# Optimization experiments

Hardware: AMD Instinct MI355X
Metric: run time of the kernel (lower is better)

The kernel has to match this reference:

```python
import jax, jax.numpy as jnp
import numpy as np

FEAT = 1024
HID = 512
DK = 256
N = 8192
KMAX = 8
K_LIST = (2, 4, 8)


def setup_inputs() -> dict:
    key = jax.random.key(0)
    ks = jax.random.split(key, 10)
    def glorot(k, shape):
        lim = np.sqrt(6.0 / (shape[0] + shape[1]))
        return jax.random.uniform(k, shape, jnp.float32, -lim, lim)
    return {
        "input_tensor": jax.random.normal(ks[0], (N, FEAT), jnp.float32),
        "sp_matrix": jax.random.randint(ks[1], (N, KMAX + 1), 0, N, jnp.int64 if jax.config.jax_enable_x64 else jnp.int32),
        "W1": glorot(ks[2], (FEAT, HID)),
        "b1": jnp.zeros((HID,), jnp.float32),
        "Wq": glorot(ks[3], (HID, DK)),
        "Wk": glorot(ks[4], (HID, DK)),
        "Wv": glorot(ks[5], (HID, DK)),
        "bv": jnp.zeros((DK,), jnp.float32),
        "Wout": glorot(ks[6], (DK, 2)),
        "bout": jnp.zeros((2,), jnp.float32),
    }


def reference(input_tensor, sp_matrix, W1, b1, Wq, Wk, Wv, bv, Wout, bout):
    # fc1: Dense(512, relu)
    dense = jax.nn.relu(input_tensor @ W1 + b1)            # [n, 512]
    # CustomAttention: scaled QK^T over the whole bag
    q = dense @ Wq                                          # [n, 256]
    k = dense @ Wk                                          # [n, 256]
    attn = (q @ k.T) / jnp.sqrt(jnp.float32(DK))            # [n, n]
    value = dense @ Wv + bv                                 # [n, 256]
    pools = []
    for kk in K_LIST:
        idx = sp_matrix[:, : kk + 1]                        # [n, kk+1]
        # sparse adjacency * attention, row-sum == gather attn[i, idx[i,j]] and sum over j
        a_raw = jnp.take_along_axis(attn, idx, axis=1).sum(axis=1)  # [n]
        alpha = jax.nn.softmax(a_raw)                       # [n]
        pools.append(alpha[:, None] * value)                # [n, 256]
    spp = jnp.concatenate(pools, axis=0)                    # [3n, 256]
    # Last_Sigmoid (subtyping=True): sum-pool -> dense -> softmax
    logits = spp.sum(axis=0, keepdims=True) @ Wout + bout   # [1, 2]
    return jax.nn.softmax(logits, axis=-1)
```

## Files before the change

kernel.cpp:

```cpp
#include <hip/hip_runtime.h>
#include <hip/hip_bf16.h>
#include <math.h>

#define FEAT 1024
#define HID  512
#define DK   256
#define NROWS 8192

typedef __attribute__((ext_vector_type(8))) short short8;
typedef __attribute__((ext_vector_type(4))) float floatx4;

__device__ __forceinline__ unsigned short f2bf(float x) {
    union { float f; unsigned u; } u;
    u.f = x;
    unsigned r = u.u;
    r += 0x7fffu + ((r >> 16) & 1u);
    return (unsigned short)(r >> 16);
}
__device__ __forceinline__ float bf2f(unsigned short x) {
    union { unsigned u; float f; } u;
    u.u = ((unsigned)x) << 16;
    return u.f;
}

__device__ __forceinline__ void gld_lds16(const unsigned short* g, unsigned short* l) {
    __builtin_amdgcn_global_load_lds(
        (__attribute__((address_space(1))) void*)(void*)g,
        (__attribute__((address_space(3))) void*)l,
        16, 0, 0);
}

__global__ __launch_bounds__(256) void prep_kernel(
    const float* __restrict__ X, const float* __restrict__ W1,
    const float* __restrict__ Wq, const float* __restrict__ Wk,
    const float* __restrict__ Wv,
    unsigned short* __restrict__ Xb, unsigned short* __restrict__ W1T,
    unsigned short* __restrict__ WqT, unsigned short* __restrict__ WkT,
    unsigned short* __restrict__ WvT,
    float* __restrict__ P, float* __restrict__ Z)
{
    const int b = blockIdx.x;
    const int tid = threadIdx.x;

    if (b == 0) {
        for (int i = tid; i < 3 * DK; i += 256) P[i] = 0.f;
        if (tid < 3) Z[tid] = 0.f;
    }
    if (b < 8192) {
        int i = b * 256 + tid;
        float4 v = ((const float4*)X)[i];
        ushort4 o;
        o.x = f2bf(v.x); o.y = f2bf(v.y); o.z = f2bf(v.z); o.w = f2bf(v.w);
        ((ushort4*)Xb)[i] = o;
        return;
    }
    int t = b - 8192;
    const float* in; unsigned short* outp; int K, N, tn, tk;
    if (t < 512) {
        in = W1; outp = W1T; K = FEAT; N = HID; tn = t & 15; tk = t >> 4;
    } else {
        t -= 512;
        int z = t >> 7, r = t & 127;
        K = HID; N = DK; tn = r & 7; tk = r >> 3;
        in   = (z == 0) ? Wq  : (z == 1) ? Wk  : Wv;
        outp = (z == 0) ? WqT : (z == 1) ? WkT : WvT;
    }
    __shared__ float tt[32][33];
    const int tx = tid & 31, ty = tid >> 5;
    const int n0 = tn * 32, k0 = tk * 32;
    #pragma unroll
    for (int i2 = ty; i2 < 32; i2 += 8)
        tt[i2][tx] = in[(size_t)(k0 + i2) * N + (n0 + tx)];
    __syncthreads();
    #pragma unroll
    for (int i2 = ty; i2 < 32; i2 += 8)
        outp[(size_t)(n0 + i2) * K + (k0 + tx)] = f2bf(tt[tx][i2]);
}

__global__ __launch_bounds__(256) void gemm_mfma(
    const unsigned short* __restrict__ A,
    const unsigned short* __restrict__ BT0, const unsigned short* __restrict__ BT1,
    const unsigned short* __restrict__ BT2,
    const float* __restrict__ bias0, const float* __restrict__ bias1,
    const float* __restrict__ bias2,
    unsigned short* __restrict__ C0, unsigned short* __restrict__ C1,
    unsigned short* __restrict__ C2,
    int N, int K, int relu)
{
    const unsigned short* BT = (blockIdx.z == 0) ? BT0 : (blockIdx.z == 1) ? BT1 : BT2;
    const float* bias        = (blockIdx.z == 0) ? bias0 : (blockIdx.z == 1) ? bias1 : bias2;
    unsigned short* C        = (blockIdx.z == 0) ? C0 : (blockIdx.z == 1) ? C1 : C2;

    __shared__ __align__(16) unsigned short As[64 * 32];
    __shared__ __align__(16) unsigned short Bs[128 * 32];

    const int tid  = threadIdx.x;
    const int lane = tid & 63;
    const int wid  = tid >> 6;
    const int wm = wid >> 1, wn = wid & 1;
    const int m0 = blockIdx.y * 64, n0 = blockIdx.x * 128;

    const int rowA = tid >> 2, gA = tid & 3;
    const int sgA = gA ^ ((rowA >> 1) & 3);
    const unsigned short* Ap = A + (size_t)(m0 + rowA) * K + sgA * 8;

    const int idx0 = tid, idx1 = tid + 256;
    const int rowB0 = idx0 >> 2, gB0 = idx0 & 3;
    const int rowB1 = idx1 >> 2, gB1 = idx1 & 3;
    const int sgB0 = gB0 ^ ((rowB0 >> 1) & 3);
    const int sgB1 = gB1 ^ ((rowB1 >> 1) & 3);
    const unsigned short* Bp0 = BT + (size_t)(n0 + rowB0) * K + sgB0 * 8;
    const unsigned short* Bp1 = BT + (size_t)(n0 + rowB1) * K + sgB1 * 8;

    char* AsB = (char*)As;
    char* BsB = (char*)Bs;
    const int ldsA  = wid * 1024;
    const int ldsB0 = wid * 1024;
    const int ldsB1 = wid * 1024 + 4096;

    const int gr = lane >> 4;
    int aoff[2], boff[4];
    #pragma unroll
    for (int i = 0; i < 2; ++i) {
        int ra = wm * 32 + i * 16 + (lane & 15);
        aoff[i] = ra * 64 + ((gr ^ ((ra >> 1) & 3)) * 16);
    }
    #pragma unroll
    for (int j = 0; j < 4; ++j) {
        int rb = wn * 64 + j * 16 + (lane & 15);
        boff[j] = rb * 64 + ((gr ^ ((rb >> 1) & 3)) * 16);
    }

    floatx4 acc[2][4];
    #pragma unroll
    for (int i = 0; i < 2; ++i)
        #pragma unroll
        for (int j = 0; j < 4; ++j)
            acc[i][j] = (floatx4){0.f, 0.f, 0.f, 0.f};

    for (int kt = 0; kt < K; kt += 32) {
        gld_lds16(Ap  + kt, (unsigned short*)(AsB + ldsA));
        gld_lds16(Bp0 + kt, (unsigned short*)(BsB + ldsB0));
        gld_lds16(Bp1 + kt, (unsigned short*)(BsB + ldsB1));
        __syncthreads();

        short8 af[2], bfr[4];
        #pragma unroll
        for (int i = 0; i < 2; ++i) af[i] = *(const short8*)(AsB + aoff[i]);
        #pragma unroll
        for (int j = 0; j < 4; ++j) bfr[j] = *(const short8*)(BsB + boff[j]);
        #pragma unroll
        for (int i = 0; i < 2; ++i)
            #pragma unroll
            for (int j = 0; j < 4; ++j)
                acc[i][j] = __builtin_amdgcn_mfma_f32_16x16x32_bf16(
                    af[i], bfr[j], acc[i][j], 0, 0, 0);
        __syncthreads();
    }

    #pragma unroll
    for (int i = 0; i < 2; ++i) {
        int rbase = m0 + wm * 32 + i * 16 + (lane >> 4) * 4;
        #pragma unroll
        for (int j = 0; j < 4; ++j) {
            int c = n0 + wn * 64 + j * 16 + (lane & 15);
            float bb = bias ? bias[c] : 0.f;
            #pragma unroll
            for (int r = 0; r < 4; ++r) {
                float v = acc[i][j][r] + bb;
                if (relu) v = fmaxf(v, 0.f);
                C[(size_t)(rbase + r) * N + c] = f2bf(v);
            }
        }
    }
}

__global__ __launch_bounds__(256) void gather_attn(
    const unsigned short* __restrict__ Q, const unsigned short* __restrict__ Kmat,
    const int* __restrict__ sp, float* __restrict__ a_raw,
    float* __restrict__ mxp)
{
    const int lane = threadIdx.x & 63;
    const int wid  = threadIdx.x >> 6;
    const int i = blockIdx.x * 4 + wid;

    ushort4 qr = *(const ushort4*)(Q + (size_t)i * DK + lane * 4);
    float4 q = make_float4(bf2f(qr.x), bf2f(qr.y), bf2f(qr.z), bf2f(qr.w));
    float4 ks = make_float4(0.f, 0.f, 0.f, 0.f);

    float mloc[3];
    int sel = 0;
    #pragma unroll
    for (int j = 0; j <= 8; ++j) {
        int r = sp[i * 9 + j];
        ushort4 kr = *(const ushort4*)(Kmat + (size_t)r * DK + lane * 4);
        ks.x += bf2f(kr.x); ks.y += bf2f(kr.y);
        ks.z += bf2f(kr.z); ks.w += bf2f(kr.w);
        if (j == 2 || j == 4 || j == 8) {
            float d = q.x * ks.x + q.y * ks.y + q.z * ks.z + q.w * ks.w;
            #pragma unroll
            for (int off = 32; off; off >>= 1) d += __shfl_xor(d, off);
            d *= 0.0625f;
            if (lane == 0) a_raw[sel * NROWS + i] = d;
            mloc[sel] = d;
            ++sel;
        }
    }

    __shared__ float sm[3][4];
    if (lane == 0) {
        sm[0][wid] = mloc[0]; sm[1][wid] = mloc[1]; sm[2][wid] = mloc[2];
    }
    __syncthreads();
    if (threadIdx.x < 3) {
        float m = fmaxf(fmaxf(sm[threadIdx.x][0], sm[threadIdx.x][1]),
                        fmaxf(sm[threadIdx.x][2], sm[threadIdx.x][3]));
        mxp[threadIdx.x * 2048 + blockIdx.x] = m;
    }
}

#define RPB 64
__global__ __launch_bounds__(256) void pool_kernel(
    const float* __restrict__ a_raw, const float* __restrict__ mxp,
    const unsigned short* __restrict__ V, float* __restrict__ P,
    float* __restrict__ Z)
{
    const int r0 = blockIdx.x * RPB;
    const int t = threadIdx.x;

    __shared__ float red[3][256];
    __shared__ float e[3][RPB];

    float m0 = -INFINITY, m1 = -INFINITY, m2 = -INFINITY;
    #pragma unroll
    for (int k = 0; k < 8; ++k) {
        int idx = t + k * 256;
        m0 = fmaxf(m0, mxp[idx]);
        m1 = fmaxf(m1, mxp[2048 + idx]);
        m2 = fmaxf(m2, mxp[4096 + idx]);
    }
    red[0][t] = m0; red[1][t] = m1; red[2][t] = m2;
    __syncthreads();
    for (int st = 128; st; st >>= 1) {
        if (t < st) {
            red[0][t] = fmaxf(red[0][t], red[0][t + st]);
            red[1][t] = fmaxf(red[1][t], red[1][t + st]);
            red[2][t] = fmaxf(red[2][t], red[2][t + st]);
        }
        __syncthreads();
    }
    m0 = red[0][0]; m1 = red[1][0]; m2 = red[2][0];

    float z0 = 0.f, z1 = 0.f, z2 = 0.f;
    if (t < RPB) {
        z0 = expf(a_raw[0 * NROWS + r0 + t] - m0);
        z1 = expf(a_raw[1 * NROWS + r0 + t] - m1);
        z2 = expf(a_raw[2 * NROWS + r0 + t] - m2);
        e[0][t] = z0; e[1][t] = z1; e[2][t] = z2;
    }
    __syncthreads();

    float a0 = 0.f, a1 = 0.f, a2 = 0.f;
    for (int r = 0; r < RPB; ++r) {
        float v = bf2f(V[(size_t)(r0 + r) * DK + t]);
        a0 = fmaf(e[0][r], v, a0);
        a1 = fmaf(e[1][r], v, a1);
        a2 = fmaf(e[2][r], v, a2);
    }
    atomicAdd(&P[0 * DK + t], a0);
    atomicAdd(&P[1 * DK + t], a1);
    atomicAdd(&P[2 * DK + t], a2);

    #pragma unroll
    for (int off = 32; off; off >>= 1) {
        z0 += __shfl_xor(z0, off); z1 += __shfl_xor(z1, off); z2 += __shfl_xor(z2, off);
    }
    if (t == 0) {
        atomicAdd(&Z[0], z0); atomicAdd(&Z[1], z1); atomicAdd(&Z[2], z2);
    }
}

__global__ __launch_bounds__(256) void final_kernel(
    const float* __restrict__ P, const float* __restrict__ Z,
    const float* __restrict__ Wout, const float* __restrict__ bout,
    float* __restrict__ out)
{
    const int t = threadIdx.x;
    float s = P[t] / Z[0] + P[DK + t] / Z[1] + P[2 * DK + t] / Z[2];
    __shared__ float s0[256], s1[256];
    s0[t] = s * Wout[t * 2 + 0];
    s1[t] = s * Wout[t * 2 + 1];
    __syncthreads();
    for (int st = 128; st; st >>= 1) {
        if (t < st) { s0[t] += s0[t + st]; s1[t] += s1[t + st]; }
        __syncthreads();
    }
    if (t == 0) {
        float a = s0[0] + bout[0], b = s1[0] + bout[1];
        float mm = fmaxf(a, b);
        float ea = expf(a - mm), eb = expf(b - mm);
        float inv = 1.f / (ea + eb);
        out[0] = ea * inv;
        out[1] = eb * inv;
    }
}

extern "C" void kernel_launch(void* const* d_in, const int* in_sizes, int n_in,
                              void* d_out, int out_size, void* d_ws, size_t ws_size,
                              hipStream_t stream)
{
    const float* X    = (const float*)d_in[0];
    const int*   sp   = (const int*)  d_in[1];
    const float* W1   = (const float*)d_in[2];
    const float* b1   = (const float*)d_in[3];
    const float* Wq   = (const float*)d_in[4];
    const float* Wk   = (const float*)d_in[5];
    const float* Wv   = (const float*)d_in[6];
    const float* bv   = (const float*)d_in[7];
    const float* Wout = (const float*)d_in[8];
    const float* bout = (const float*)d_in[9];
    float* out = (float*)d_out;

    char* w = (char*)d_ws;
    unsigned short* dense_b = (unsigned short*)(w);
    unsigned short* W1T     = (unsigned short*)(w +  8388608);
    unsigned short* WqT     = (unsigned short*)(w +  9437184);
    unsigned short* WkT     = (unsigned short*)(w +  9699328);
    unsigned short* WvT     = (unsigned short*)(w +  9961472);
    float* a_raw            = (float*)(w + 10223616);
    float* P                = (float*)(w + 10321920);
    float* Z                = P + 3 * DK;
    float* mxp              = (float*)(w + 10330112);
    unsigned short* Qb      = (unsigned short*)(w + 10485760);
    unsigned short* Kb      = (unsigned short*)(w + 14680064);
    unsigned short* Vb      = (unsigned short*)(w + 18874368);
    unsigned short* Xb      = (unsigned short*)(w + 10485760);

    prep_kernel<<<8192 + 512 + 384, 256, 0, stream>>>(
        X, W1, Wq, Wk, Wv, Xb, W1T, WqT, WkT, WvT, P, Z);

    gemm_mfma<<<dim3(HID / 128, NROWS / 64, 1), 256, 0, stream>>>(
        Xb, W1T, nullptr, nullptr, b1, nullptr, nullptr,
        dense_b, nullptr, nullptr, HID, FEAT, 1);

    gemm_mfma<<<dim3(DK / 128, NROWS / 64, 3), 256, 0, stream>>>(
        dense_b, WqT, WkT, WvT, nullptr, nullptr, bv,
        Qb, Kb, Vb, DK, HID, 0);

    gather_attn<<<NROWS / 4, 256, 0, stream>>>(Qb, Kb, sp, a_raw, mxp);
    pool_kernel<<<NROWS / RPB, 256, 0, stream>>>(a_raw, mxp, Vb, P, Z);
    final_kernel<<<1, 256, 0, stream>>>(P, Z, Wout, bout, out);
}
```

Measured before the change: 71.54 us.

## Fuse X bf16 cast into GEMM, double-buffer LDS, fold final kernel into pool

Removes the separate pass that converts X to bf16. The first GEMM now reads fp32 X directly and converts it to bf16 while staging into LDS, which saves a full write and read of the bf16 copy. The GEMM now double-buffers its LDS tiles so the next tile's loads overlap the current tile's MFMAs, with one barrier per iteration. The final reduction kernel is folded into pool_kernel through a last-block atomic counter, saving a launch at the cost of threadfence and atomic reads.

```diff
diff --git a/kernel.cpp b/kernel.cpp
--- a/kernel.cpp
+++ b/kernel.cpp
@@ -30,14 +30,21 @@
         16, 0, 0);
 }
 
+__device__ __forceinline__ short8 cast8(float4 a, float4 b) {
+    short8 r;
+    r[0] = (short)f2bf(a.x); r[1] = (short)f2bf(a.y);
+    r[2] = (short)f2bf(a.z); r[3] = (short)f2bf(a.w);
+    r[4] = (short)f2bf(b.x); r[5] = (short)f2bf(b.y);
+    r[6] = (short)f2bf(b.z); r[7] = (short)f2bf(b.w);
+    return r;
+}
+
 __global__ __launch_bounds__(256) void prep_kernel(
-    const float* __restrict__ X, const float* __restrict__ W1,
-    const float* __restrict__ Wq, const float* __restrict__ Wk,
-    const float* __restrict__ Wv,
-    unsigned short* __restrict__ Xb, unsigned short* __restrict__ W1T,
-    unsigned short* __restrict__ WqT, unsigned short* __restrict__ WkT,
-    unsigned short* __restrict__ WvT,
-    float* __restrict__ P, float* __restrict__ Z)
+    const float* __restrict__ W1, const float* __restrict__ Wq,
+    const float* __restrict__ Wk, const float* __restrict__ Wv,
+    unsigned short* __restrict__ W1T, unsigned short* __restrict__ WqT,
+    unsigned short* __restrict__ WkT, unsigned short* __restrict__ WvT,
+    float* __restrict__ P, float* __restrict__ Z, unsigned* __restrict__ counter)
 {
     const int b = blockIdx.x;
     const int tid = threadIdx.x;
@@ -45,16 +52,10 @@
     if (b == 0) {
         for (int i = tid; i < 3 * DK; i += 256) P[i] = 0.f;
         if (tid < 3) Z[tid] = 0.f;
-    }
-    if (b < 8192) {
-        int i = b * 256 + tid;
-        float4 v = ((const float4*)X)[i];
-        ushort4 o;
-        o.x = f2bf(v.x); o.y = f2bf(v.y); o.z = f2bf(v.z); o.w = f2bf(v.w);
-        ((ushort4*)Xb)[i] = o;
-        return;
-    }
-    int t = b - 8192;
+        if (tid == 0) *counter = 0u;
+    }
+
+    int t = b;
     const float* in; unsigned short* outp; int K, N, tn, tk;
     if (t < 512) {
         in = W1; outp = W1T; K = FEAT; N = HID; tn = t & 15; tk = t >> 4;
@@ -77,8 +78,9 @@
         outp[(size_t)(n0 + i2) * K + (k0 + tx)] = f2bf(tt[tx][i2]);
 }
 
+template<int A_F32>
 __global__ __launch_bounds__(256) void gemm_mfma(
-    const unsigned short* __restrict__ A,
+    const void* __restrict__ Av,
     const unsigned short* __restrict__ BT0, const unsigned short* __restrict__ BT1,
     const unsigned short* __restrict__ BT2,
     const float* __restrict__ bias0, const float* __restrict__ bias1,
@@ -91,8 +93,8 @@
     const float* bias        = (blockIdx.z == 0) ? bias0 : (blockIdx.z == 1) ? bias1 : bias2;
     unsigned short* C        = (blockIdx.z == 0) ? C0 : (blockIdx.z == 1) ? C1 : C2;
 
-    __shared__ __align__(16) unsigned short As[64 * 32];
-    __shared__ __align__(16) unsigned short Bs[128 * 32];
+    __shared__ __align__(16) unsigned short As[2][64 * 32];
+    __shared__ __align__(16) unsigned short Bs[2][128 * 32];
 
     const int tid  = threadIdx.x;
     const int lane = tid & 63;
@@ -102,22 +104,17 @@
 
     const int rowA = tid >> 2, gA = tid & 3;
     const int sgA = gA ^ ((rowA >> 1) & 3);
-    const unsigned short* Ap = A + (size_t)(m0 + rowA) * K + sgA * 8;
-
-    const int idx0 = tid, idx1 = tid + 256;
-    const int rowB0 = idx0 >> 2, gB0 = idx0 & 3;
+    const float*          ApF = (const float*)Av + (size_t)(m0 + rowA) * K + gA * 8;
+    const unsigned short* ApB = (const unsigned short*)Av + (size_t)(m0 + rowA) * K + sgA * 8;
+
+    const int idx1 = tid + 256;
+    const int rowB0 = tid >> 2,  gB0 = tid & 3;
     const int rowB1 = idx1 >> 2, gB1 = idx1 & 3;
     const int sgB0 = gB0 ^ ((rowB0 >> 1) & 3);
     const int sgB1 = gB1 ^ ((rowB1 >> 1) & 3);
     const unsigned short* Bp0 = BT + (size_t)(n0 + rowB0) * K + sgB0 * 8;
     const unsigned short* Bp1 = BT + (size_t)(n0 + rowB1) * K + sgB1 * 8;
 
-    char* AsB = (char*)As;
-    char* BsB = (char*)Bs;
-    const int ldsA  = wid * 1024;
-    const int ldsB0 = wid * 1024;
-    const int ldsB1 = wid * 1024 + 4096;
-
     const int gr = lane >> 4;
     int aoff[2], boff[4];
     #pragma unroll
@@ -138,24 +135,66 @@
         for (int j = 0; j < 4; ++j)
             acc[i][j] = (floatx4){0.f, 0.f, 0.f, 0.f};
 
-    for (int kt = 0; kt < K; kt += 32) {
-        gld_lds16(Ap  + kt, (unsigned short*)(AsB + ldsA));
-        gld_lds16(Bp0 + kt, (unsigned short*)(BsB + ldsB0));
-        gld_lds16(Bp1 + kt, (unsigned short*)(BsB + ldsB1));
-        __syncthreads();
-
+    if (A_F32) {
+        float4 a0 = *(const float4*)(ApF);
+        float4 a1 = *(const float4*)(ApF + 4);
+        gld_lds16(Bp0, (unsigned short*)((char*)Bs[0] + wid * 1024));
+        gld_lds16(Bp1, (unsigned short*)((char*)Bs[0] + wid * 1024 + 4096));
+        *(short8*)((char*)As[0] + rowA * 64 + sgA * 16) = cast8(a0, a1);
+    } else {
+        gld_lds16(ApB, (unsigned short*)((char*)As[0] + wid * 1024));
+        gld_lds16(Bp0, (unsigned short*)((char*)Bs[0] + wid * 1024));
+        gld_lds16(Bp1, (unsigned short*)((char*)Bs[0] + wid * 1024 + 4096));
+    }
+    __syncthreads();
+
+    int cur = 0;
+    for (int kt = 32; kt < K; kt += 32) {
+        float4 na, nb;
+        if (A_F32) {
+            na = *(const float4*)(ApF + kt);
+            nb = *(const float4*)(ApF + kt + 4);
+        } else {
+            gld_lds16(ApB + kt, (unsigned short*)((char*)As[cur ^ 1] + wid * 1024));
+        }
+        gld_lds16(Bp0 + kt, (unsigned short*)((char*)Bs[cur ^ 1] + wid * 1024));
+        gld_lds16(Bp1 + kt, (unsigned short*)((char*)Bs[cur ^ 1] + wid * 1024 + 4096));
+
+        const char* AsC = (const char*)As[cur];
+        const char* BsC = (const char*)Bs[cur];
         short8 af[2], bfr[4];
         #pragma unroll
-        for (int i = 0; i < 2; ++i) af[i] = *(const short8*)(AsB + aoff[i]);
-        #pragma unroll
-        for (int j = 0; j < 4; ++j) bfr[j] = *(const short8*)(BsB + boff[j]);
+        for (int i = 0; i < 2; ++i) af[i] = *(const short8*)(AsC + aoff[i]);
+        #pragma unroll
+        for (int j = 0; j < 4; ++j) bfr[j] = *(const short8*)(BsC + boff[j]);
         #pragma unroll
         for (int i = 0; i < 2; ++i)
             #pragma unroll
             for (int j = 0; j < 4; ++j)
                 acc[i][j] = __builtin_amdgcn_mfma_f32_16x16x32_bf16(
                     af[i], bfr[j], acc[i][j], 0, 0, 0);
+
+        if (A_F32)
+            *(short8*)((char*)As[cur ^ 1] + rowA * 64 + sgA * 16) = cast8(na, nb);
+
         __syncthreads();
+        cur ^= 1;
+    }
+
+    {
+        const char* AsC = (const char*)As[cur];
+        const char* BsC = (const char*)Bs[cur];
+        short8 af[2], bfr[4];
+        #pragma unroll
+        for (int i = 0; i < 2; ++i) af[i] = *(const short8*)(AsC + aoff[i]);
+        #pragma unroll
+        for (int j = 0; j < 4; ++j) bfr[j] = *(const short8*)(BsC + boff[j]);
+        #pragma unroll
+        for (int i = 0; i < 2; ++i)
+            #pragma unroll
+            for (int j = 0; j < 4; ++j)
+                acc[i][j] = __builtin_amdgcn_mfma_f32_16x16x32_bf16(
+                    af[i], bfr[j], acc[i][j], 0, 0, 0);
     }
 
     #pragma unroll
@@ -223,13 +262,17 @@
 __global__ __launch_bounds__(256) void pool_kernel(
     const float* __restrict__ a_raw, const float* __restrict__ mxp,
     const unsigned short* __restrict__ V, float* __restrict__ P,
-    float* __restrict__ Z)
+    float* __restrict__ Z, unsigned* __restrict__ counter,
+    const float* __restrict__ Wout, const float* __restrict__ bout,
+    float* __restrict__ out)
 {
     const int r0 = blockIdx.x * RPB;
     const int t = threadIdx.x;
 
     __shared__ float red[3][256];
     __shared__ float e[3][RPB];
+    __shared__ unsigned rank;
+    __shared__ float zz[3];
 
     float m0 = -INFINITY, m1 = -INFINITY, m2 = -INFINITY;
     #pragma unroll
@@ -278,30 +321,36 @@
     if (t == 0) {
         atomicAdd(&Z[0], z0); atomicAdd(&Z[1], z1); atomicAdd(&Z[2], z2);
     }
-}
-
-__global__ __launch_bounds__(256) void final_kernel(
-    const float* __restrict__ P, const float* __restrict__ Z,
-    const float* __restrict__ Wout, const float* __restrict__ bout,
-    float* __restrict__ out)
-{
-    const int t = threadIdx.x;
-    float s = P[t] / Z[0] + P[DK + t] / Z[1] + P[2 * DK + t] / Z[2];
-    __shared__ float s0[256], s1[256];
-    s0[t] = s * Wout[t * 2 + 0];
-    s1[t] = s * Wout[t * 2 + 1];
-    __syncthreads();
-    for (int st = 128; st; st >>= 1) {
-        if (t < st) { s0[t] += s0[t + st]; s1[t] += s1[t + st]; }
+
+    __threadfence();
+    if (t == 0) rank = atomicAdd(counter, 1u);
+    __syncthreads();
+    if (rank == gridDim.x - 1) {
+        __threadfence();
+        if (t < 3) zz[t] = atomicAdd(&Z[t], 0.0f);
         __syncthreads();
-    }
-    if (t == 0) {
-        float a = s0[0] + bout[0], b = s1[0] + bout[1];
-        float mm = fmaxf(a, b);
-        float ea = expf(a - mm), eb = expf(b - mm);
-        float inv = 1.f / (ea + eb);
-        out[0] = ea * inv;
-        out[1] = eb * inv;
+        float p0 = atomicAdd(&P[0 * DK + t], 0.0f);
+        float p1 = atomicAdd(&P[1 * DK + t], 0.0f);
+        float p2 = atomicAdd(&P[2 * DK + t], 0.0f);
+        float s = p0 / zz[0] + p1 / zz[1] + p2 / zz[2];
+        red[0][t] = s * Wout[t * 2 + 0];
+        red[1][t] = s * Wout[t * 2 + 1];
+        __syncthreads();
+        for (int st = 128; st; st >>= 1) {
+            if (t < st) {
+                red[0][t] += red[0][t + st];
+                red[1][t] += red[1][t + st];
+            }
+            __syncthreads();
+        }
+        if (t == 0) {
+            float a = red[0][0] + bout[0], b = red[1][0] + bout[1];
+            float mm = fmaxf(a, b);
+            float ea = expf(a - mm), eb = expf(b - mm);
+            float inv = 1.f / (ea + eb);
+            out[0] = ea * inv;
+            out[1] = eb * inv;
+        }
     }
 }
 
@@ -330,24 +379,24 @@
     float* a_raw            = (float*)(w + 10223616);
     float* P                = (float*)(w + 10321920);
     float* Z                = P + 3 * DK;
+    unsigned* counter       = (unsigned*)(Z + 3);
     float* mxp              = (float*)(w + 10330112);
     unsigned short* Qb      = (unsigned short*)(w + 10485760);
     unsigned short* Kb      = (unsigned short*)(w + 14680064);
     unsigned short* Vb      = (unsigned short*)(w + 18874368);
-    unsigned short* Xb      = (unsigned short*)(w + 10485760);
-
-    prep_kernel<<<8192 + 512 + 384, 256, 0, stream>>>(
-        X, W1, Wq, Wk, Wv, Xb, W1T, WqT, WkT, WvT, P, Z);
-
-    gemm_mfma<<<dim3(HID / 128, NROWS / 64, 1), 256, 0, stream>>>(
-        Xb, W1T, nullptr, nullptr, b1, nullptr, nullptr,
+
+    prep_kernel<<<896, 256, 0, stream>>>(
+        W1, Wq, Wk, Wv, W1T, WqT, WkT, WvT, P, Z, counter);
+
+    gemm_mfma<1><<<dim3(HID / 128, NROWS / 64, 1), 256, 0, stream>>>(
+        X, W1T, nullptr, nullptr, b1, nullptr, nullptr,
         dense_b, nullptr, nullptr, HID, FEAT, 1);
 
-    gemm_mfma<<<dim3(DK / 128, NROWS / 64, 3), 256, 0, stream>>>(
+    gemm_mfma<0><<<dim3(DK / 128, NROWS / 64, 3), 256, 0, stream>>>(
         dense_b, WqT, WkT, WvT, nullptr, nullptr, bv,
         Qb, Kb, Vb, DK, HID, 0);
 
     gather_attn<<<NROWS / 4, 256, 0, stream>>>(Qb, Kb, sp, a_raw, mxp);
-    pool_kernel<<<NROWS / RPB, 256, 0, stream>>>(a_raw, mxp, Vb, P, Z);
-    final_kernel<<<1, 256, 0, stream>>>(P, Z, Wout, bout, out);
-}
+    pool_kernel<<<NROWS / RPB, 256, 0, stream>>>(
+        a_raw, mxp, Vb, P, Z, counter, Wout, bout, out);
+}
```

Measured after the change: 89.22 us. 1.25x slower.

## Remap GEMM blocks to XCD-aware 1D grid and fuse final reduction into pool

Applied to the files above, without the earlier changes.

Each GEMM launch becomes a 1D grid whose block index is decoded so that blocks sharing an A row-tile land on the same XCD (blockIdx & 7). The goal is better L2 reuse of the A operand across N tiles and Q/K/V outputs. Separately, final_kernel is removed: pool_kernel uses an atomic completion counter so the last block reads P and Z and computes the output softmax, saving one kernel launch. The last-block pattern depends on fences and atomic reads for correctness, and it adds a serial tail to one block.

```diff
diff --git a/kernel.cpp b/kernel.cpp
--- a/kernel.cpp
+++ b/kernel.cpp
@@ -37,7 +37,7 @@
     unsigned short* __restrict__ Xb, unsigned short* __restrict__ W1T,
     unsigned short* __restrict__ WqT, unsigned short* __restrict__ WkT,
     unsigned short* __restrict__ WvT,
-    float* __restrict__ P, float* __restrict__ Z)
+    float* __restrict__ P, float* __restrict__ Z, unsigned* __restrict__ counter)
 {
     const int b = blockIdx.x;
     const int tid = threadIdx.x;
@@ -45,6 +45,7 @@
     if (b == 0) {
         for (int i = tid; i < 3 * DK; i += 256) P[i] = 0.f;
         if (tid < 3) Z[tid] = 0.f;
+        if (tid == 0) *counter = 0u;
     }
     if (b < 8192) {
         int i = b * 256 + tid;
@@ -85,11 +86,20 @@
     const float* __restrict__ bias2,
     unsigned short* __restrict__ C0, unsigned short* __restrict__ C1,
     unsigned short* __restrict__ C2,
-    int N, int K, int relu)
-{
-    const unsigned short* BT = (blockIdx.z == 0) ? BT0 : (blockIdx.z == 1) ? BT1 : BT2;
-    const float* bias        = (blockIdx.z == 0) ? bias0 : (blockIdx.z == 1) ? bias1 : bias2;
-    unsigned short* C        = (blockIdx.z == 0) ? C0 : (blockIdx.z == 1) ? C1 : C2;
+    int N, int K, int relu, int nbx, int nz)
+{
+    const int nbxe = nbx * nz;
+    const int xcd = blockIdx.x & 7;
+    const int j   = blockIdx.x >> 3;
+    const int grp = j / nbxe;
+    const int sub = j - grp * nbxe;
+    const int by  = xcd + (grp << 3);
+    const int bx  = sub % nbx;
+    const int z   = sub / nbx;
+
+    const unsigned short* BT = (z == 0) ? BT0 : (z == 1) ? BT1 : BT2;
+    const float* bias        = (z == 0) ? bias0 : (z == 1) ? bias1 : bias2;
+    unsigned short* C        = (z == 0) ? C0 : (z == 1) ? C1 : C2;
 
     __shared__ __align__(16) unsigned short As[64 * 32];
     __shared__ __align__(16) unsigned short Bs[128 * 32];
@@ -98,14 +108,14 @@
     const int lane = tid & 63;
     const int wid  = tid >> 6;
     const int wm = wid >> 1, wn = wid & 1;
-    const int m0 = blockIdx.y * 64, n0 = blockIdx.x * 128;
+    const int m0 = by * 64, n0 = bx * 128;
 
     const int rowA = tid >> 2, gA = tid & 3;
     const int sgA = gA ^ ((rowA >> 1) & 3);
     const unsigned short* Ap = A + (size_t)(m0 + rowA) * K + sgA * 8;
 
-    const int idx0 = tid, idx1 = tid + 256;
-    const int rowB0 = idx0 >> 2, gB0 = idx0 & 3;
+    const int idx1 = tid + 256;
+    const int rowB0 = tid >> 2,  gB0 = tid & 3;
     const int rowB1 = idx1 >> 2, gB1 = idx1 & 3;
     const int sgB0 = gB0 ^ ((rowB0 >> 1) & 3);
     const int sgB1 = gB1 ^ ((rowB1 >> 1) & 3);
@@ -126,17 +136,17 @@
         aoff[i] = ra * 64 + ((gr ^ ((ra >> 1) & 3)) * 16);
     }
     #pragma unroll
-    for (int j = 0; j < 4; ++j) {
-        int rb = wn * 64 + j * 16 + (lane & 15);
-        boff[j] = rb * 64 + ((gr ^ ((rb >> 1) & 3)) * 16);
+    for (int jj = 0; jj < 4; ++jj) {
+        int rb = wn * 64 + jj * 16 + (lane & 15);
+        boff[jj] = rb * 64 + ((gr ^ ((rb >> 1) & 3)) * 16);
     }
 
     floatx4 acc[2][4];
     #pragma unroll
     for (int i = 0; i < 2; ++i)
         #pragma unroll
-        for (int j = 0; j < 4; ++j)
-            acc[i][j] = (floatx4){0.f, 0.f, 0.f, 0.f};
+        for (int jj = 0; jj < 4; ++jj)
+            acc[i][jj] = (floatx4){0.f, 0.f, 0.f, 0.f};
 
     for (int kt = 0; kt < K; kt += 32) {
         gld_lds16(Ap  + kt, (unsigned short*)(AsB + ldsA));
@@ -148,13 +158,13 @@
         #pragma unroll
         for (int i = 0; i < 2; ++i) af[i] = *(const short8*)(AsB + aoff[i]);
         #pragma unroll
-        for (int j = 0; j < 4; ++j) bfr[j] = *(const short8*)(BsB + boff[j]);
+        for (int jj = 0; jj < 4; ++jj) bfr[jj] = *(const short8*)(BsB + boff[jj]);
         #pragma unroll
         for (int i = 0; i < 2; ++i)
             #pragma unroll
-            for (int j = 0; j < 4; ++j)
-                acc[i][j] = __builtin_amdgcn_mfma_f32_16x16x32_bf16(
-                    af[i], bfr[j], acc[i][j], 0, 0, 0);
+            for (int jj = 0; jj < 4; ++jj)
+                acc[i][jj] = __builtin_amdgcn_mfma_f32_16x16x32_bf16(
+                    af[i], bfr[jj], acc[i][jj], 0, 0, 0);
         __syncthreads();
     }
 
@@ -162,12 +172,12 @@
     for (int i = 0; i < 2; ++i) {
         int rbase = m0 + wm * 32 + i * 16 + (lane >> 4) * 4;
         #pragma unroll
-        for (int j = 0; j < 4; ++j) {
-            int c = n0 + wn * 64 + j * 16 + (lane & 15);
+        for (int jj = 0; jj < 4; ++jj) {
+            int c = n0 + wn * 64 + jj * 16 + (lane & 15);
             float bb = bias ? bias[c] : 0.f;
             #pragma unroll
             for (int r = 0; r < 4; ++r) {
-                float v = acc[i][j][r] + bb;
+                float v = acc[i][jj][r] + bb;
                 if (relu) v = fmaxf(v, 0.f);
                 C[(size_t)(rbase + r) * N + c] = f2bf(v);
             }
@@ -223,13 +233,17 @@
 __global__ __launch_bounds__(256) void pool_kernel(
     const float* __restrict__ a_raw, const float* __restrict__ mxp,
     const unsigned short* __restrict__ V, float* __restrict__ P,
-    float* __restrict__ Z)
+    float* __restrict__ Z, unsigned* __restrict__ counter,
+    const float* __restrict__ Wout, const float* __restrict__ bout,
+    float* __restrict__ out)
 {
     const int r0 = blockIdx.x * RPB;
     const int t = threadIdx.x;
 
     __shared__ float red[3][256];
     __shared__ float e[3][RPB];
+    __shared__ unsigned rank;
+    __shared__ float zz[3];
 
     float m0 = -INFINITY, m1 = -INFINITY, m2 = -INFINITY;
     #pragma unroll
@@ -278,30 +292,36 @@
     if (t == 0) {
         atomicAdd(&Z[0], z0); atomicAdd(&Z[1], z1); atomicAdd(&Z[2], z2);
     }
-}
-
-__global__ __launch_bounds__(256) void final_kernel(
-    const float* __restrict__ P, const float* __restrict__ Z,
-    const float* __restrict__ Wout, const float* __restrict__ bout,
-    float* __restrict__ out)
-{
-    const int t = threadIdx.x;
-    float s = P[t] / Z[0] + P[DK + t] / Z[1] + P[2 * DK + t] / Z[2];
-    __shared__ float s0[256], s1[256];
-    s0[t] = s * Wout[t * 2 + 0];
-    s1[t] = s * Wout[t * 2 + 1];
-    __syncthreads();
-    for (int st = 128; st; st >>= 1) {
-        if (t < st) { s0[t] += s0[t + st]; s1[t] += s1[t + st]; }
-        __syncthreads();
-    }
-    if (t == 0) {
-        float a = s0[0] + bout[0], b = s1[0] + bout[1];
-        float mm = fmaxf(a, b);
-        float ea = expf(a - mm), eb = expf(b - mm);
-        float inv = 1.f / (ea + eb);
-        out[0] = ea * inv;
-        out[1] = eb * inv;
+
+    __threadfence();
+    if (t == 0) rank = atomicAdd(counter, 1u);
+    __syncthreads();
+    if (rank == gridDim.x - 1) {
+        __threadfence();
+        if (t < 3) zz[t] = atomicAdd(&Z[t], 0.0f);
+        __syncthreads();
+        float p0 = atomicAdd(&P[0 * DK + t], 0.0f);
+        float p1 = atomicAdd(&P[1 * DK + t], 0.0f);
+        float p2 = atomicAdd(&P[2 * DK + t], 0.0f);
+        float s = p0 / zz[0] + p1 / zz[1] + p2 / zz[2];
+        red[0][t] = s * Wout[t * 2 + 0];
+        red[1][t] = s * Wout[t * 2 + 1];
+        __syncthreads();
+        for (int st = 128; st; st >>= 1) {
+            if (t < st) {
+                red[0][t] += red[0][t + st];
+                red[1][t] += red[1][t + st];
+            }
+            __syncthreads();
+        }
+        if (t == 0) {
+            float a = red[0][0] + bout[0], b = red[1][0] + bout[1];
+            float mm = fmaxf(a, b);
+            float ea = expf(a - mm), eb = expf(b - mm);
+            float inv = 1.f / (ea + eb);
+            out[0] = ea * inv;
+            out[1] = eb * inv;
+        }
     }
 }
 
@@ -330,6 +350,7 @@
     float* a_raw            = (float*)(w + 10223616);
     float* P                = (float*)(w + 10321920);
     float* Z                = P + 3 * DK;
+    unsigned* counter       = (unsigned*)(Z + 3);
     float* mxp              = (float*)(w + 10330112);
     unsigned short* Qb      = (unsigned short*)(w + 10485760);
     unsigned short* Kb      = (unsigned short*)(w + 14680064);
@@ -337,17 +358,17 @@
     unsigned short* Xb      = (unsigned short*)(w + 10485760);
 
     prep_kernel<<<8192 + 512 + 384, 256, 0, stream>>>(
-        X, W1, Wq, Wk, Wv, Xb, W1T, WqT, WkT, WvT, P, Z);
-
-    gemm_mfma<<<dim3(HID / 128, NROWS / 64, 1), 256, 0, stream>>>(
+        X, W1, Wq, Wk, Wv, Xb, W1T, WqT, WkT, WvT, P, Z, counter);
+
+    gemm_mfma<<<512, 256, 0, stream>>>(
         Xb, W1T, nullptr, nullptr, b1, nullptr, nullptr,
-        dense_b, nullptr, nullptr, HID, FEAT, 1);
-
-    gemm_mfma<<<dim3(DK / 128, NROWS / 64, 3), 256, 0, stream>>>(
+        dense_b, nullptr, nullptr, HID, FEAT, 1, 4, 1);
+
+    gemm_mfma<<<768, 256, 0, stream>>>(
         dense_b, WqT, WkT, WvT, nullptr, nullptr, bv,
-        Qb, Kb, Vb, DK, HID, 0);
+        Qb, Kb, Vb, DK, HID, 0, 2, 3);
 
     gather_attn<<<NROWS / 4, 256, 0, stream>>>(Qb, Kb, sp, a_raw, mxp);
-    pool_kernel<<<NROWS / RPB, 256, 0, stream>>>(a_raw, mxp, Vb, P, Z);
-    final_kernel<<<1, 256, 0, stream>>>(P, Z, Wout, bout, out);
-}
+    pool_kernel<<<NROWS / RPB, 256, 0, stream>>>(
+        a_raw, mxp, Vb, P, Z, counter, Wout, bout, out);
+}
```

Measured after the change: 78.31 us. +9.5%, slower.
